# Optimization experiments

Hardware: AMD Instinct MI355X
Metric: run time of the kernel (lower is better)

The kernel has to match this reference:

```python
import jax, jax.numpy as jnp
import numpy as np

MD = 4            # max_displacement
PATCH = 2 * MD + 1  # 9 displacements per axis (kernel_size=1, stride=1, pad=0)


def setup_inputs() -> dict:
    key = jax.random.key(0)
    k1, k2 = jax.random.split(key)
    feat1 = jax.random.normal(k1, (4, 256, 64, 64), jnp.float32)
    feat2 = jax.random.normal(k2, (4, 256, 64, 64), jnp.float32)
    return {"feat1": feat1, "feat2": feat2}


def _correlation(feat1, feat2, md):
    """SpatialCorrelationSampler with kernel_size=1, patch=2*md+1, stride=1, pad=0.
    out[b,di,dj,y,x] = sum_c feat1[b,c,y,x] * feat2[b,c,y+di-md, x+dj-md] (zero outside).
    Returns (B, P, P, H, W)."""
    B, C, H, W = feat1.shape
    P = 2 * md + 1
    f2p = jnp.pad(feat2, ((0, 0), (0, 0), (md, md), (md, md)))
    # fixed small loop over 81 displacements (not a data-dim loop)
    slices = [
        jnp.sum(feat1 * jax.lax.dynamic_slice(f2p, (0, 0, di, dj), (B, C, H, W)), axis=1)
        for di in range(P) for dj in range(P)
    ]
    return jnp.stack(slices, axis=1).reshape(B, P, P, H, W)


def _remap(cv, md):
    """Vectorized equivalent of remap_cost_volume's python double loop:
    out[b, r+di-md, c+dj-md, r, c] = cv[b, di, dj, r, c] for in-bounds targets."""
    B, P, _, H, W = cv.shape
    d = jnp.arange(P) - md
    r = jnp.arange(H)
    c = jnp.arange(W)
    tr = d[:, None] + r[None, :]            # (P, H) target rows
    tc = d[:, None] + c[None, :]            # (P, W) target cols
    vr = (tr >= 0) & (tr < H)
    vc = (tc >= 0) & (tc < W)
    TR = jnp.clip(tr, 0, H - 1)[:, None, :, None]   # (P,1,H,1)
    TC = jnp.clip(tc, 0, W - 1)[None, :, None, :]   # (1,P,1,W)
    mask = vr[:, None, :, None] & vc[None, :, None, :]  # (P,P,H,W)
    vals = cv * mask.astype(cv.dtype)                   # (B,P,P,H,W)
    R = r[None, None, :, None]
    Cc = c[None, None, None, :]
    TRb, TCb, Rb, Cb = jnp.broadcast_arrays(TR, TC, R, Cc)  # (P,P,H,W)
    out = jnp.zeros((B, H, W, H, W), cv.dtype)
    out = out.at[:, TRb, TCb, Rb, Cb].add(vals)
    return out


def reference(feat1, feat2):
    cv = _correlation(feat1, feat2, MD)      # (B,P,P,H,W)
    B = cv.shape[0]
    H, W = cv.shape[-2], cv.shape[-1]
    remapped = _remap(cv, MD)                # (B,H,W,H,W)
    return remapped.reshape(B, H * W, H, W)  # final .view(B,-1,rows,cols)
```

## Files before the change

### kernel.cpp

```cpp
#include <hip/hip_runtime.h>

#define MD 4
#define PATCH 9
#define NBAND 256
#define NZERO 1024
#define BT 1024

template<int ND>
__device__ __forceinline__ void band_core(
    const float* __restrict__ f1base,
    const float (* __restrict__ sF2)[72],
    int ty, int dy0, int lane,
    float acc[3][PATCH])
{
    int yoff[ND];
#pragma unroll
    for (int i = 0; i < ND; ++i) {
        int y = ty + dy0 + i - MD;
        y = y < 0 ? 0 : (y > 63 ? 63 : y);
        yoff[i] = y * 64;
    }

#pragma unroll 2
    for (int c = 0; c < 64; ++c) {
        const float* f1c = f1base + (size_t)c * 4096;
        float f1v[ND];
#pragma unroll
        for (int i = 0; i < ND; ++i)
            f1v[i] = f1c[yoff[i]];
        const float* wp = &sF2[c][lane];
        float sh[PATCH];
#pragma unroll
        for (int dxi = 0; dxi < PATCH; ++dxi)
            sh[dxi] = wp[8 - dxi];
#pragma unroll
        for (int i = 0; i < ND; ++i)
#pragma unroll
            for (int dxi = 0; dxi < PATCH; ++dxi)
                acc[i][dxi] = fmaf(f1v[i], sh[dxi], acc[i][dxi]);
    }
}

__global__ __launch_bounds__(BT, 8) void cv_kernel(
    const float* __restrict__ f1,
    const float* __restrict__ f2,
    float* __restrict__ out)
{
    const int tid = threadIdx.x;

    if (blockIdx.x >= NBAND) {
        float4* o4 = (float4*)out;
        const float4 z4 = make_float4(0.f, 0.f, 0.f, 0.f);
        const int total4 = 4 * 4096 * 64 * 16;
        const int stride = NZERO * BT;
        for (int i = (blockIdx.x - NBAND) * BT + tid; i < total4; i += stride) {
            int y  = (i >> 4) & 63;
            int ty = (i >> 16) & 63;
            int dy = y - ty;
            if (dy < -MD || dy > MD)
                o4[i] = z4;
        }
        return;
    }

    const int bty = blockIdx.x;
    const int b   = bty >> 6;
    const int ty  = bty & 63;
    const int lane = tid & 63;
    const int w    = tid >> 6;
    const int cq   = w >> 2;
    const int dyg  = w & 3;
    const int dy0  = dyg * 2;
    const int nd   = (dyg == 3) ? 3 : 2;

    __shared__ float uLds[256 * 72];
    float (*sF2)[72] = (float(*)[72])uLds;

    const float4* f2g = (const float4*)f2 + (size_t)(b * 256) * 1024 + ty * 16;
#pragma unroll
    for (int k = 0; k < 4; ++k) {
        int idx = k * BT + tid;
        int cl = idx >> 4, x4 = idx & 15;
        *(float4*)&sF2[cl][4 + 4 * x4] = f2g[(size_t)cl * 1024 + x4];
    }
    if (tid < 512) {
        int cl = tid >> 1, off = (tid & 1) ? 68 : 0;
        *(float4*)&sF2[cl][off] = make_float4(0.f, 0.f, 0.f, 0.f);
    }
    __syncthreads();

    float acc[3][PATCH];
#pragma unroll
    for (int i = 0; i < 3; ++i)
#pragma unroll
        for (int j = 0; j < PATCH; ++j) acc[i][j] = 0.f;

    const float* f1b = f1 + (size_t)(b * 256 + cq * 64) * 4096 + lane;
    const float (*sF2w)[72] = &sF2[cq * 64];

    if (dyg == 3) band_core<3>(f1b, sF2w, ty, dy0, lane, acc);
    else          band_core<2>(f1b, sF2w, ty, dy0, lane, acc);

    __syncthreads();
    float (*sVals)[81] = (float(*)[81])uLds;

    if (cq == 0) {
#pragma unroll
        for (int i = 0; i < 3; ++i) {
            if (i >= nd) continue;
            int dyi = dy0 + i;
            int y = ty + dyi - MD;
            if ((unsigned)y >= 64u) continue;
#pragma unroll
            for (int dxi = 0; dxi < PATCH; ++dxi) {
                int tx = lane - (dxi - MD);
                if ((unsigned)tx < 64u)
                    sVals[tx][dyi * PATCH + dxi] = acc[i][dxi];
            }
        }
    }
    __syncthreads();
    if (cq != 0) {
#pragma unroll
        for (int i = 0; i < 3; ++i) {
            if (i >= nd) continue;
            int dyi = dy0 + i;
            int y = ty + dyi - MD;
            if ((unsigned)y >= 64u) continue;
#pragma unroll
            for (int dxi = 0; dxi < PATCH; ++dxi) {
                int tx = lane - (dxi - MD);
                if ((unsigned)tx < 64u)
                    atomicAdd(&sVals[tx][dyi * PATCH + dxi], acc[i][dxi]);
            }
        }
    }
    __syncthreads();

    float4* out4 = (float4*)(out + (size_t)(b * 4096 + ty * 64) * 4096);
    const int q4 = tid & 15;
    const int ro = tid >> 4;
    for (int rb = 0; rb < 64 * PATCH; rb += 64) {
        int row = rb + ro;
        int tx  = row / PATCH;
        int dyi = row - tx * PATCH;
        int y   = ty + dyi - MD;
        if ((unsigned)y < 64u) {
            float comp[4];
#pragma unroll
            for (int j = 0; j < 4; ++j) {
                int x  = q4 * 4 + j;
                int dx = x - tx;
                comp[j] = (dx >= -MD && dx <= MD) ? sVals[tx][dyi * PATCH + dx + MD] : 0.f;
            }
            out4[tx * 1024 + y * 16 + q4] = make_float4(comp[0], comp[1], comp[2], comp[3]);
        }
    }
}

extern "C" void kernel_launch(void* const* d_in, const int* in_sizes, int n_in,
                              void* d_out, int out_size, void* d_ws, size_t ws_size,
                              hipStream_t stream) {
    const float* f1 = (const float*)d_in[0];
    const float* f2 = (const float*)d_in[1];
    float* out = (float*)d_out;
    cv_kernel<<<NBAND + NZERO, BT, 0, stream>>>(f1, f2, out);
}
```

Measured before the change: 91.16 us.

## Split each band block into two dy halves, reorder zero blocks first, use nontemporal stores

Each (batch, row) band is now split across two blocks, one handling displacement rows 0-3 and the other rows 4-8. This doubles the number of compute blocks and cuts per-thread accumulator registers. The zero-fill blocks now get the low block indices so they are scheduled first. All output writes go through nontemporal vector stores to avoid polluting cache with the large write-only output. The trade-off is that f2 is staged into LDS twice per band and the f1 loads are repeated across the two halves.

```diff
diff --git a/kernel.cpp b/kernel.cpp
--- a/kernel.cpp
+++ b/kernel.cpp
@@ -2,16 +2,24 @@
 
 #define MD 4
 #define PATCH 9
-#define NBAND 256
 #define NZERO 1024
+#define NBANDB 512
 #define BT 1024
+
+typedef float f4v __attribute__((ext_vector_type(4)));
+
+__device__ __forceinline__ void nt_store4(float* p, float a, float b, float c, float d)
+{
+    f4v v = {a, b, c, d};
+    __builtin_nontemporal_store(v, (f4v*)p);
+}
 
 template<int ND>
 __device__ __forceinline__ void band_core(
     const float* __restrict__ f1base,
     const float (* __restrict__ sF2)[72],
     int ty, int dy0, int lane,
-    float acc[3][PATCH])
+    float acc[2][PATCH])
 {
     int yoff[ND];
 #pragma unroll
@@ -21,59 +29,56 @@
         yoff[i] = y * 64;
     }
 
+    if constexpr (ND == 1) {
+#pragma unroll 4
+        for (int c = 0; c < 64; ++c) {
+            const float* f1c = f1base + (size_t)c * 4096;
+            float f1v = f1c[yoff[0]];
+            const float* wp = &sF2[c][lane];
+            float sh[PATCH];
+#pragma unroll
+            for (int dxi = 0; dxi < PATCH; ++dxi)
+                sh[dxi] = wp[8 - dxi];
+#pragma unroll
+            for (int dxi = 0; dxi < PATCH; ++dxi)
+                acc[0][dxi] = fmaf(f1v, sh[dxi], acc[0][dxi]);
+        }
+    } else {
 #pragma unroll 2
-    for (int c = 0; c < 64; ++c) {
-        const float* f1c = f1base + (size_t)c * 4096;
-        float f1v[ND];
-#pragma unroll
-        for (int i = 0; i < ND; ++i)
-            f1v[i] = f1c[yoff[i]];
-        const float* wp = &sF2[c][lane];
-        float sh[PATCH];
-#pragma unroll
-        for (int dxi = 0; dxi < PATCH; ++dxi)
-            sh[dxi] = wp[8 - dxi];
-#pragma unroll
-        for (int i = 0; i < ND; ++i)
+        for (int c = 0; c < 64; ++c) {
+            const float* f1c = f1base + (size_t)c * 4096;
+            float f1v[ND];
+#pragma unroll
+            for (int i = 0; i < ND; ++i)
+                f1v[i] = f1c[yoff[i]];
+            const float* wp = &sF2[c][lane];
+            float sh[PATCH];
 #pragma unroll
             for (int dxi = 0; dxi < PATCH; ++dxi)
-                acc[i][dxi] = fmaf(f1v[i], sh[dxi], acc[i][dxi]);
-    }
-}
-
-__global__ __launch_bounds__(BT, 8) void cv_kernel(
-    const float* __restrict__ f1,
-    const float* __restrict__ f2,
-    float* __restrict__ out)
-{
-    const int tid = threadIdx.x;
-
-    if (blockIdx.x >= NBAND) {
-        float4* o4 = (float4*)out;
-        const float4 z4 = make_float4(0.f, 0.f, 0.f, 0.f);
-        const int total4 = 4 * 4096 * 64 * 16;
-        const int stride = NZERO * BT;
-        for (int i = (blockIdx.x - NBAND) * BT + tid; i < total4; i += stride) {
-            int y  = (i >> 4) & 63;
-            int ty = (i >> 16) & 63;
-            int dy = y - ty;
-            if (dy < -MD || dy > MD)
-                o4[i] = z4;
-        }
-        return;
-    }
-
-    const int bty = blockIdx.x;
-    const int b   = bty >> 6;
-    const int ty  = bty & 63;
+                sh[dxi] = wp[8 - dxi];
+#pragma unroll
+            for (int i = 0; i < ND; ++i)
+#pragma unroll
+                for (int dxi = 0; dxi < PATCH; ++dxi)
+                    acc[i][dxi] = fmaf(f1v[i], sh[dxi], acc[i][dxi]);
+        }
+    }
+}
+
+template<int HALF>
+__device__ __forceinline__ void do_band(
+    const float* __restrict__ f1, const float* __restrict__ f2,
+    float* __restrict__ out, float* uLds, int b, int ty, int tid)
+{
+    constexpr int DY0 = HALF ? 4 : 0;
+    constexpr int NR  = HALF ? 5 : 4;
     const int lane = tid & 63;
     const int w    = tid >> 6;
     const int cq   = w >> 2;
     const int dyg  = w & 3;
-    const int dy0  = dyg * 2;
-    const int nd   = (dyg == 3) ? 3 : 2;
-
-    __shared__ float uLds[256 * 72];
+    const int dy0w = DY0 + dyg;
+    const int nd   = (HALF && dyg == 3) ? 2 : 1;
+
     float (*sF2)[72] = (float(*)[72])uLds;
 
     const float4* f2g = (const float4*)f2 + (size_t)(b * 256) * 1024 + ty * 16;
@@ -89,26 +94,26 @@
     }
     __syncthreads();
 
-    float acc[3][PATCH];
-#pragma unroll
-    for (int i = 0; i < 3; ++i)
+    float acc[2][PATCH];
+#pragma unroll
+    for (int i = 0; i < 2; ++i)
 #pragma unroll
         for (int j = 0; j < PATCH; ++j) acc[i][j] = 0.f;
 
     const float* f1b = f1 + (size_t)(b * 256 + cq * 64) * 4096 + lane;
     const float (*sF2w)[72] = &sF2[cq * 64];
 
-    if (dyg == 3) band_core<3>(f1b, sF2w, ty, dy0, lane, acc);
-    else          band_core<2>(f1b, sF2w, ty, dy0, lane, acc);
+    if (HALF && dyg == 3) band_core<2>(f1b, sF2w, ty, dy0w, lane, acc);
+    else                  band_core<1>(f1b, sF2w, ty, dy0w, lane, acc);
 
     __syncthreads();
     float (*sVals)[81] = (float(*)[81])uLds;
 
     if (cq == 0) {
 #pragma unroll
-        for (int i = 0; i < 3; ++i) {
+        for (int i = 0; i < 2; ++i) {
             if (i >= nd) continue;
-            int dyi = dy0 + i;
+            int dyi = dy0w + i;
             int y = ty + dyi - MD;
             if ((unsigned)y >= 64u) continue;
 #pragma unroll
@@ -122,9 +127,9 @@
     __syncthreads();
     if (cq != 0) {
 #pragma unroll
-        for (int i = 0; i < 3; ++i) {
+        for (int i = 0; i < 2; ++i) {
             if (i >= nd) continue;
-            int dyi = dy0 + i;
+            int dyi = dy0w + i;
             int y = ty + dyi - MD;
             if ((unsigned)y >= 64u) continue;
 #pragma unroll
@@ -137,14 +142,15 @@
     }
     __syncthreads();
 
-    float4* out4 = (float4*)(out + (size_t)(b * 4096 + ty * 64) * 4096);
+    float* outb = out + (size_t)(b * 4096 + ty * 64) * 4096;
     const int q4 = tid & 15;
     const int ro = tid >> 4;
-    for (int rb = 0; rb < 64 * PATCH; rb += 64) {
+    for (int rb = 0; rb < 64 * NR; rb += 64) {
         int row = rb + ro;
-        int tx  = row / PATCH;
-        int dyi = row - tx * PATCH;
-        int y   = ty + dyi - MD;
+        int tx, dyi;
+        if (NR == 4) { tx = row >> 2; dyi = DY0 + (row & 3); }
+        else         { tx = row / 5;  dyi = DY0 + (row - 5 * tx); }
+        int y = ty + dyi - MD;
         if ((unsigned)y < 64u) {
             float comp[4];
 #pragma unroll
@@ -153,9 +159,41 @@
                 int dx = x - tx;
                 comp[j] = (dx >= -MD && dx <= MD) ? sVals[tx][dyi * PATCH + dx + MD] : 0.f;
             }
-            out4[tx * 1024 + y * 16 + q4] = make_float4(comp[0], comp[1], comp[2], comp[3]);
-        }
-    }
+            nt_store4(outb + (size_t)tx * 4096 + y * 64 + q4 * 4,
+                      comp[0], comp[1], comp[2], comp[3]);
+        }
+    }
+}
+
+__global__ __launch_bounds__(BT, 8) void cv_kernel(
+    const float* __restrict__ f1,
+    const float* __restrict__ f2,
+    float* __restrict__ out)
+{
+    __shared__ float uLds[256 * 72];
+    const int tid = threadIdx.x;
+
+    if (blockIdx.x < NZERO) {
+        float* o = (float*)out;
+        const int total4 = 4 * 4096 * 64 * 16;
+        const int stride = NZERO * BT;
+        for (int i = blockIdx.x * BT + tid; i < total4; i += stride) {
+            int y  = (i >> 4) & 63;
+            int ty = (i >> 16) & 63;
+            int dy = y - ty;
+            if (dy < -MD || dy > MD)
+                nt_store4(o + (size_t)i * 4, 0.f, 0.f, 0.f, 0.f);
+        }
+        return;
+    }
+
+    const int bb  = blockIdx.x - NZERO;
+    const int bty = bb >> 1;
+    const int b   = bty >> 6;
+    const int ty  = bty & 63;
+
+    if (bb & 1) do_band<1>(f1, f2, out, uLds, b, ty, tid);
+    else        do_band<0>(f1, f2, out, uLds, b, ty, tid);
 }
 
 extern "C" void kernel_launch(void* const* d_in, const int* in_sizes, int n_in,
@@ -164,5 +202,5 @@
     const float* f1 = (const float*)d_in[0];
     const float* f2 = (const float*)d_in[1];
     float* out = (float*)d_out;
-    cv_kernel<<<NBAND + NZERO, BT, 0, stream>>>(f1, f2, out);
-}
+    cv_kernel<<<NZERO + NBANDB, BT, 0, stream>>>(f1, f2, out);
+}
```

After: 108.2 us. 1.19x slower.
